# Kernel optimization log

Hardware: AMD Instinct MI355X
Metric: run time of the kernel (lower is better)

## Reference

```python
import jax, jax.numpy as jnp
import numpy as np

T_STEPS, N, STATE, HID, ACT, C = 32, 64, 64, 128, 32, 96


def setup_inputs() -> dict:
    key = jax.random.key(0)
    ks = jax.random.split(key, 16)
    s = 0.05
    inp = {
        'x': jax.random.normal(ks[0], (T_STEPS, N, STATE), jnp.float32),
        'a': jax.random.normal(ks[1], (T_STEPS, N, ACT), jnp.float32),
        # GRU layer 0 (input state_dim) and layer 1 (input hidden_dim)
        'wih0': jax.random.normal(ks[2], (3 * HID, STATE), jnp.float32) * s,
        'whh0': jax.random.normal(ks[3], (3 * HID, HID), jnp.float32) * s,
        'bih0': jax.random.normal(ks[4], (3 * HID,), jnp.float32) * s,
        'bhh0': jax.random.normal(ks[5], (3 * HID,), jnp.float32) * s,
        'wih1': jax.random.normal(ks[6], (3 * HID, HID), jnp.float32) * s,
        'whh1': jax.random.normal(ks[7], (3 * HID, HID), jnp.float32) * s,
        'bih1': jax.random.normal(ks[8], (3 * HID,), jnp.float32) * s,
        'bhh1': jax.random.normal(ks[9], (3 * HID,), jnp.float32) * s,
        'w1': jax.random.normal(ks[10], (HID, HID + ACT), jnp.float32) * s,
        'b1': jax.random.normal(ks[11], (HID,), jnp.float32) * s,
        'w2': jax.random.normal(ks[12], (1, 2 * HID), jnp.float32) * s,
        'b2': jax.random.normal(ks[13], (1,), jnp.float32) * s,
        'Tm': jax.random.normal(ks[14], (HID, HID, C), jnp.float32),  # init.normal(T,0,1)
    }
    return inp


def _gru_cell(x_t, h, wih, whh, bih, bhh):
    gi = x_t @ wih.T + bih            # (N, 3H)
    gh = h @ whh.T + bhh
    i_r, i_z, i_n = jnp.split(gi, 3, axis=-1)
    h_r, h_z, h_n = jnp.split(gh, 3, axis=-1)
    r = jax.nn.sigmoid(i_r + h_r)
    z = jax.nn.sigmoid(i_z + h_z)
    n = jnp.tanh(i_n + r * h_n)
    return (1.0 - z) * n + z * h


def reference(x, a, wih0, whh0, bih0, bhh0, wih1, whh1, bih1, bhh1, w1, b1, w2, b2, Tm):
    def step(h, x_t):
        h0 = _gru_cell(x_t, h[0], wih0, whh0, bih0, bhh0)
        h1 = _gru_cell(h0, h[1], wih1, whh1, bih1, bhh1)
        return jnp.stack([h0, h1]), h1

    h_init = jnp.zeros((2, N, HID), x.dtype)
    _, p = jax.lax.scan(step, h_init, x)              # (T, N, H)

    fc1 = jax.nn.relu(jnp.concatenate([p, a], -1) @ w1.T + b1)  # (T, N, H)

    Tflat = Tm.reshape(HID, HID * C)

    def batch_discrim(xt):  # xt: (N, H)
        M = (xt @ Tflat).reshape(N, HID, C)           # (N, B, C)
        # pairwise L1 over C: (N, N, B)
        norm = jnp.abs(M[:, None] - M[None, :]).sum(-1)
        o_b = (jnp.exp(-norm).sum(0) - 1.0) / (N - 1)  # (N, B)
        return jnp.concatenate([xt, o_b], 1)          # (N, 2H)

    fc2 = jax.lax.map(batch_discrim, fc1)             # (T, N, 2H)
    prob = jax.nn.sigmoid(fc2 @ w2.T + b2)            # (T, N, 1)
    return prob
```

## Files before the change

### kernel.cpp

```cpp
#include <hip/hip_runtime.h>
#include <hip/hip_fp16.h>
#include <cstdint>

#define T_STEPS 32
#define NB 64
#define STATE 64
#define HID 128
#define ACT 32
#define CDIM 96
#define G3 (3*HID)

typedef __attribute__((ext_vector_type(8))) short short8;
typedef __attribute__((ext_vector_type(4))) float f32x4;
typedef _Float16 h2v __attribute__((ext_vector_type(2)));

__device__ __forceinline__ unsigned short f2bf(float f){
  unsigned int u = __builtin_bit_cast(unsigned int, f);
  u = u + 0x7FFFu + ((u >> 16) & 1u);
  return (unsigned short)(u >> 16);
}
__device__ __forceinline__ float bf2f(unsigned short u){
  unsigned int v = ((unsigned int)u) << 16; return __builtin_bit_cast(float, v);
}
__device__ __forceinline__ unsigned int packh2(float f0, float f1){
  return (unsigned int)__half_as_ushort(__float2half_rn(f0)) |
         ((unsigned int)__half_as_ushort(__float2half_rn(f1)) << 16);
}
__device__ __forceinline__ float sigmoidf_(float x){ return 1.0f/(1.0f + __expf(-x)); }
__device__ __forceinline__ float tanhf_(float x){ float e = __expf(2.0f*x); return (e-1.0f)/(e+1.0f); }

__device__ __forceinline__ float dot2f(float acc, unsigned int a, unsigned int b){
  h2v av = __builtin_bit_cast(h2v, a);
  h2v bv = __builtin_bit_cast(h2v, b);
  return __builtin_amdgcn_fdot2(av, bv, acc, false);
}
__device__ __forceinline__ float l1d(float acc, unsigned int ua, unsigned int ub){
  __half2 a = __builtin_bit_cast(__half2, ua);
  __half2 b = __builtin_bit_cast(__half2, ub);
  __half2 d = __habs2(__hsub2(a, b));
  h2v dv = __builtin_bit_cast(h2v, d);
  h2v ones; ones[0] = (_Float16)1.0f; ones[1] = (_Float16)1.0f;
  return __builtin_amdgcn_fdot2(dv, ones, acc, false);
}
__device__ __forceinline__ float l1d4(float acc, uint4 a, uint4 b){
  acc = l1d(acc, a.x, b.x); acc = l1d(acc, a.y, b.y);
  acc = l1d(acc, a.z, b.z); acc = l1d(acc, a.w, b.w);
  return acc;
}

__global__ void k_prep(const float* __restrict__ Tm, unsigned short* __restrict__ tmh,
                       const float* __restrict__ whh0, const float* __restrict__ whh1,
                       const float* __restrict__ w1, const float* __restrict__ wih0,
                       const float* __restrict__ wih1, const float* __restrict__ x,
                       const float* __restrict__ a,
                       unsigned int* __restrict__ whh0p, unsigned int* __restrict__ whh1p,
                       unsigned short* __restrict__ w1f, unsigned short* __restrict__ wi0f,
                       unsigned short* __restrict__ wi1f, unsigned short* __restrict__ xaf,
                       unsigned short* __restrict__ h1af){
  int tid = threadIdx.x;
  int bx = blockIdx.x;
  if (bx < 128){
    int b = bx;
    for (int e = tid; e < HID*CDIM; e += 256){
      int chunk = e / 768;
      int r1 = e - chunk*768;
      int c = r1 >> 3, h = r1 & 7;
      int k = chunk*8 + h;
      tmh[b*(HID*CDIM) + e] = f2bf(Tm[k*(HID*CDIM) + b*CDIM + c]);
    }
  } else if (bx < 132){
    for (int e = (bx-128)*256 + tid; e < 24576; e += 1024){
      int k2 = e / 384, r = e - k2*384;
      whh0p[e] = packh2(whh0[r*128 + 2*k2], whh0[r*128 + 2*k2 + 1]);
      whh1p[e] = packh2(whh1[r*128 + 2*k2], whh1[r*128 + 2*k2 + 1]);
    }
  } else if (bx < 136){
    for (int e = (bx-132)*256 + tid; e < 20480; e += 1024){
      int kc = e >> 10, rem = e & 1023;
      int col = rem >> 3, j = rem & 7;
      w1f[e] = f2bf(w1[col*160 + kc*8 + j]);
    }
  } else if (bx < 140){
    for (int e = (bx-136)*256 + tid; e < 24576; e += 1024){
      int kc = e / 3072, rem = e - kc*3072;
      int col = rem >> 3, kl = rem & 7;
      wi0f[e] = f2bf(wih0[col*64 + kc*8 + kl]);
    }
  } else if (bx < 144){
    for (int e = (bx-140)*256 + tid; e < 49152; e += 1024){
      int kc = e / 3072, rem = e - kc*3072;
      int col = rem >> 3, kl = rem & 7;
      wi1f[e] = f2bf(wih1[col*128 + kc*8 + kl]);
    }
  } else if (bx < 156){
    for (int e = (bx-144)*256 + tid; e < 131072; e += 3072){
      int t = e >> 12, rem = e & 4095;
      int ntile = rem >> 10, rem2 = rem & 1023;
      int kc = rem2 >> 7, nl = (rem2 >> 3) & 15, kl = rem2 & 7;
      int n = ntile*16 + nl, k = kc*8 + kl;
      xaf[e] = f2bf(x[t*4096 + n*64 + k]);
    }
  } else {
    for (int e = (bx-156)*256 + tid; e < 65536; e += 3072){
      int t = e >> 11, rem = e & 2047;
      int n = rem >> 5, c = rem & 31;
      int pos = t*10240 + (n>>4)*2560 + (16 + (c>>3))*128 + (n&15)*8 + (c&7);
      h1af[pos] = f2bf(a[t*(NB*ACT) + n*ACT + c]);
    }
  }
}

template<int KK, int TSU>
__global__ __launch_bounds__(256) void k_gi(const unsigned short* __restrict__ af,
                                            const unsigned short* __restrict__ wf,
                                            const float* __restrict__ bias,
                                            float* __restrict__ gig){
  int t = blockIdx.x, by = blockIdx.y, tid = threadIdx.x;
  int wave = tid >> 6, lane = tid & 63, m = lane & 15, quad = lane >> 4;
  const uint4* A4 = (const uint4*)af;
  const uint4* B4 = (const uint4*)wf;
  uint4 av[KK];
  #pragma unroll
  for (int kk = 0; kk < KK; kk++) av[kk] = A4[t*TSU + wave*(TSU/4) + (kk*4+quad)*16 + m];
  f32x4 acc[6];
  #pragma unroll
  for (int i = 0; i < 6; i++) acc[i] = (f32x4)(0.0f);
  #pragma unroll
  for (int kk = 0; kk < KK; kk++){
    short8 a = __builtin_bit_cast(short8, av[kk]);
    #pragma unroll
    for (int ntl = 0; ntl < 6; ntl++){
      int nt = by*6 + ntl;
      uint4 bv = B4[(kk*4+quad)*384 + nt*16 + m];
      acc[ntl] = __builtin_amdgcn_mfma_f32_16x16x32_bf16(a, __builtin_bit_cast(short8, bv), acc[ntl], 0, 0, 0);
    }
  }
  #pragma unroll
  for (int ntl = 0; ntl < 6; ntl++){
    int col = (by*6+ntl)*16 + m;
    float bv = bias[col];
    #pragma unroll
    for (int rr = 0; rr < 4; rr++){
      int n = wave*16 + quad*4 + rr;
      gig[(t*NB + n)*G3 + col] = acc[ntl][rr] + bv;
    }
  }
}

template<int TS, int NS>
__global__ __launch_bounds__(768, 3) void k_rec(const unsigned int* __restrict__ whhp,
                                                const float* __restrict__ bhh,
                                                const float* __restrict__ gig,
                                                unsigned short* __restrict__ haf){
  __shared__ __align__(16) unsigned int hl[64];
  __shared__ float A0[G3];
  int n = blockIdx.x, tid = threadIdx.x;
  int r = tid >> 1, kh = tid & 1;
  unsigned int wh[32];
  #pragma unroll
  for (int i = 0; i < 32; i++) wh[i] = whhp[(kh*32 + i)*384 + r];
  float bh = (kh == 0) ? bhh[r] : 0.0f;
  if (tid < 64) hl[tid] = 0u;
  float g_r = 0.0f, g_z = 0.0f, g_n = 0.0f, hprev = 0.0f;
  if (tid < HID){
    const float* gp = gig + n*G3 + tid;
    g_r = gp[0]; g_z = gp[HID]; g_n = gp[2*HID];
  }
  __syncthreads();
  const uint4* h4 = (const uint4*)hl;
  for (int t = 0; t < T_STEPS; t++){
    float gh = bh;
    #pragma unroll
    for (int g = 0; g < 2; g++){
      uint4 hv[4];
      #pragma unroll
      for (int j = 0; j < 4; j++) hv[j] = h4[kh*8 + g*4 + j];
      #pragma unroll
      for (int j = 0; j < 4; j++){
        gh = dot2f(gh, wh[g*16 + j*4 + 0], hv[j].x);
        gh = dot2f(gh, wh[g*16 + j*4 + 1], hv[j].y);
        gh = dot2f(gh, wh[g*16 + j*4 + 2], hv[j].z);
        gh = dot2f(gh, wh[g*16 + j*4 + 3], hv[j].w);
      }
    }
    gh += __shfl_xor(gh, 1);
    if (kh == 0) A0[r] = gh;
    __syncthreads();
    if (tid < HID){
      float cr = g_r, cz = g_z, cn = g_n;
      int tn2 = (t+1 < T_STEPS) ? t+1 : t;
      const float* gp = gig + (tn2*NB + n)*G3 + tid;
      g_r = gp[0]; g_z = gp[HID]; g_n = gp[2*HID];
      float rg = sigmoidf_(cr + A0[tid]);
      float z  = sigmoidf_(cz + A0[tid+HID]);
      float nn = tanhf_   (cn + rg*A0[tid+2*HID]);
      float hn = (1.0f - z)*nn + z*hprev;
      hprev = hn;
      ((__half*)hl)[tid] = __float2half_rn(hn);
      haf[t*TS + (n>>4)*NS + (tid>>3)*128 + (n&15)*8 + (tid&7)] = f2bf(hn);
    }
    __syncthreads();
  }
}

__global__ __launch_bounds__(256) void k_fc1(const unsigned short* __restrict__ h1af,
                                             const unsigned short* __restrict__ w1f,
                                             const float* __restrict__ b1,
                                             unsigned short* __restrict__ fc1h){
  __shared__ float b1s[128];
  int t = blockIdx.x, tid = threadIdx.x;
  int wave = tid >> 6, lane = tid & 63, m = lane & 15, quad = lane >> 4;
  if (tid < 128) b1s[tid] = b1[tid];
  const uint4* A4 = (const uint4*)(h1af + t*10240);
  const uint4* B4 = (const uint4*)w1f;
  f32x4 acc[8];
  #pragma unroll
  for (int i = 0; i < 8; i++) acc[i] = (f32x4)(0.0f);
  #pragma unroll
  for (int ks = 0; ks < 5; ks++){
    uint4 av = A4[wave*320 + (ks*4 + quad)*16 + m];
    short8 avs = __builtin_bit_cast(short8, av);
    #pragma unroll
    for (int nt = 0; nt < 8; nt++){
      uint4 bv = B4[(ks*4 + quad)*128 + nt*16 + m];
      acc[nt] = __builtin_amdgcn_mfma_f32_16x16x32_bf16(avs, __builtin_bit_cast(short8, bv), acc[nt], 0, 0, 0);
    }
  }
  __syncthreads();
  #pragma unroll
  for (int nt = 0; nt < 8; nt++){
    float bj = b1s[nt*16 + m];
    #pragma unroll
    for (int rr = 0; rr < 4; rr++){
      float v = fmaxf(acc[nt][rr] + bj, 0.0f);
      fc1h[t*8192 + wave*2048 + (nt*2 + (m>>3))*128 + (quad*4 + rr)*8 + (m&7)] = f2bf(v);
    }
  }
}

__global__ __launch_bounds__(256) void k_disc(const unsigned short* __restrict__ fc1h,
                                              const unsigned short* __restrict__ tmh,
                                              float* __restrict__ O){
  __shared__ __align__(16) __half Mh[64*104];
  __shared__ float ps[64*18];
  int b = blockIdx.x;
  int tid = threadIdx.x;
  int wave = tid >> 6, lane = tid & 63, m = lane & 15, quad = lane >> 4;
  const uint4* Bg = (const uint4*)(tmh + b*(CDIM*HID));
  #pragma unroll 1
  for (int tt = 0; tt < 4; tt++){
    int t = blockIdx.y*4 + tt;
    const uint4* Ag = (const uint4*)(fc1h + t*8192);
    uint4 a4[4];
    #pragma unroll
    for (int kk = 0; kk < 4; kk++) a4[kk] = Ag[wave*256 + (kk*4 + quad)*16 + m];
    f32x4 acc[6];
    #pragma unroll
    for (int i = 0; i < 6; i++) acc[i] = (f32x4)(0.0f);
    #pragma unroll
    for (int kk = 0; kk < 4; kk++){
      short8 av = __builtin_bit_cast(short8, a4[kk]);
      #pragma unroll
      for (int nt = 0; nt < 6; nt++){
        uint4 b4 = Bg[(kk*4 + quad)*96 + nt*16 + m];
        acc[nt] = __builtin_amdgcn_mfma_f32_16x16x32_bf16(av, __builtin_bit_cast(short8, b4), acc[nt], 0, 0, 0);
      }
    }
    __syncthreads();
    #pragma unroll
    for (int nt = 0; nt < 6; nt++){
      #pragma unroll
      for (int rr = 0; rr < 4; rr++){
        Mh[(rr*16 + wave*4 + quad)*104 + nt*16 + m] = __float2half(acc[nt][rr]);
      }
    }
    __syncthreads();
    const uint4* M4 = (const uint4*)Mh;
    if (tid < 240){
      int chalf = tid & 1, tp = tid >> 1;
      int rnd = tp >> 3, slot = tp & 7;
      int ta, tb;
      if (slot == 0){ ta = 15; tb = rnd; }
      else {
        ta = rnd + slot;      if (ta >= 15) ta -= 15;
        tb = rnd + 15 - slot; if (tb >= 15) tb -= 15;
      }
      float facc[16];
      #pragma unroll
      for (int p = 0; p < 16; p++) facc[p] = 0.0f;
      auto doChunk = [&](int c){
        int ch = chalf*6 + c;
        uint4 av[4], bv[4];
        #pragma unroll
        for (int s = 0; s < 4; s++){
          av[s] = M4[(s*16 + ta)*13 + ch];
          bv[s] = M4[(s*16 + tb)*13 + ch];
        }
        #pragma unroll
        for (int i = 0; i < 4; i++)
          #pragma unroll
          for (int j = 0; j < 4; j++)
            facc[i*4+j] = l1d4(facc[i*4+j], av[i], bv[j]);
      };
      doChunk(0); doChunk(1);
      bool big1 = true;
      #pragma unroll
      for (int p = 0; p < 16; p++) big1 = big1 && (facc[p] > 14.0f);
      if (!big1){
        doChunk(2); doChunk(3);
        bool big2 = true;
        #pragma unroll
        for (int p = 0; p < 16; p++) big2 = big2 && (facc[p] > 14.0f);
        if (!big2){ doChunk(4); doChunk(5); }
      }
      float tot[16];
      #pragma unroll
      for (int p = 0; p < 16; p++) tot[p] = facc[p] + __shfl_xor(facc[p], 1);
      if (chalf == 0){
        #pragma unroll
        for (int i = 0; i < 4; i++){
          float s = 0.0f;
          #pragma unroll
          for (int j = 0; j < 4; j++) s += __expf(-tot[i*4+j]);
          ps[(ta*4 + i)*18 + tb] = s;
        }
      } else {
        #pragma unroll
        for (int j = 0; j < 4; j++){
          float s = 0.0f;
          #pragma unroll
          for (int i = 0; i < 4; i++) s += __expf(-tot[i*4+j]);
          ps[(tb*4 + j)*18 + ta] = s;
        }
      }
    } else {
      int ta = tid - 240;
      float f6[6];
      #pragma unroll
      for (int p = 0; p < 6; p++) f6[p] = 0.0f;
      auto doChunkS = [&](int ch){
        uint4 rv[4];
        #pragma unroll
        for (int s = 0; s < 4; s++) rv[s] = M4[(s*16 + ta)*13 + ch];
        f6[0] = l1d4(f6[0], rv[0], rv[1]);
        f6[1] = l1d4(f6[1], rv[0], rv[2]);
        f6[2] = l1d4(f6[2], rv[0], rv[3]);
        f6[3] = l1d4(f6[3], rv[1], rv[2]);
        f6[4] = l1d4(f6[4], rv[1], rv[3]);
        f6[5] = l1d4(f6[5], rv[2], rv[3]);
      };
      doChunkS(0); doChunkS(1); doChunkS(2);
      bool big1 = true;
      #pragma unroll
      for (int p = 0; p < 6; p++) big1 = big1 && (f6[p] > 14.0f);
      if (!big1){
        doChunkS(3); doChunkS(4); doChunkS(5);
        bool big2 = true;
        #pragma unroll
        for (int p = 0; p < 6; p++) big2 = big2 && (f6[p] > 14.0f);
        if (!big2){
          doChunkS(6); doChunkS(7); doChunkS(8);
          doChunkS(9); doChunkS(10); doChunkS(11);
        }
      }
      float e01 = __expf(-f6[0]), e02 = __expf(-f6[1]), e03 = __expf(-f6[2]);
      float e12 = __expf(-f6[3]), e13 = __expf(-f6[4]), e23 = __expf(-f6[5]);
      ps[(ta*4 + 0)*18 + ta] = e01 + e02 + e03;
      ps[(ta*4 + 1)*18 + ta] = e01 + e12 + e13;
      ps[(ta*4 + 2)*18 + ta] = e02 + e12 + e23;
      ps[(ta*4 + 3)*18 + ta] = e03 + e13 + e23;
    }
    __syncthreads();
    if (tid < NB){
      float s = 0.0f;
      #pragma unroll
      for (int k = 0; k < 16; k++) s += ps[tid*18 + k];
      O[(t*HID + b)*NB + tid] = s*(1.0f/63.0f);
    }
  }
}

__global__ __launch_bounds__(256) void k_final(const unsigned short* __restrict__ fc1h,
                                               const float* __restrict__ O,
                                               const float* __restrict__ w2, const float* __restrict__ b2,
                                               float* __restrict__ out){
  __shared__ float ol[NB*HID];
  __shared__ unsigned short fr[8192];
  __shared__ float wl[2*HID + 2];
  int t = blockIdx.x, tid = threadIdx.x;
  for (int i = tid; i < NB*HID; i += 256) ol[i] = O[t*NB*HID + i];
  const uint4* Fg = (const uint4*)(fc1h + t*8192);
  for (int i = tid; i < 1024; i += 256) ((uint4*)fr)[i] = Fg[i];
  if (tid < 2*HID) wl[tid] = w2[tid];
  if (tid == 0) wl[2*HID] = b2[0];
  __syncthreads();
  if (tid < NB){
    float acc = wl[2*HID];
    int base = (tid>>4)*2048 + (tid&15)*8;
    #pragma unroll 8
    for (int j = 0; j < HID; j++) acc += bf2f(fr[base + (j>>3)*128 + (j&7)])*wl[j];
    #pragma unroll 8
    for (int b = 0; b < HID; b++) acc += ol[b*NB + tid]*wl[HID + b];
    out[t*NB + tid] = sigmoidf_(acc);
  }
}

extern "C" void kernel_launch(void* const* d_in, const int* in_sizes, int n_in,
                              void* d_out, int out_size, void* d_ws, size_t ws_size,
                              hipStream_t stream){
  const float* x    = (const float*)d_in[0];
  const float* a    = (const float*)d_in[1];
  const float* wih0 = (const float*)d_in[2];
  const float* whh0 = (const float*)d_in[3];
  const float* bih0 = (const float*)d_in[4];
  const float* bhh0 = (const float*)d_in[5];
  const float* wih1 = (const float*)d_in[6];
  const float* whh1 = (const float*)d_in[7];
  const float* bih1 = (const float*)d_in[8];
  const float* bhh1 = (const float*)d_in[9];
  const float* w1   = (const float*)d_in[10];
  const float* b1   = (const float*)d_in[11];
  const float* w2   = (const float*)d_in[12];
  const float* b2   = (const float*)d_in[13];
  const float* Tm   = (const float*)d_in[14];
  float* ws = (float*)d_ws;
  float* Ows = ws;
  unsigned int* whh0p = (unsigned int*)(ws + 262144);
  unsigned int* whh1p = (unsigned int*)(ws + 286720);
  unsigned short* tmh  = (unsigned short*)(ws + 311296);
  unsigned short* fc1h = (unsigned short*)(ws + 1097728);
  unsigned short* h1af = (unsigned short*)(ws + 1228800);
  unsigned short* w1f  = (unsigned short*)(ws + 1392640);
  unsigned short* xaf  = (unsigned short*)(ws + 1402880);
  unsigned short* wi0f = (unsigned short*)(ws + 1468416);
  unsigned short* wi1f = (unsigned short*)(ws + 1480704);
  unsigned short* h0af = (unsigned short*)(ws + 1505280);
  float* gig = ws + 1636352;
  float* out = (float*)d_out;

  k_prep<<<dim3(168), dim3(256), 0, stream>>>(Tm, tmh, whh0, whh1, w1, wih0, wih1, x, a,
                                              whh0p, whh1p, w1f, wi0f, wi1f, xaf, h1af);
  k_gi<2, 512><<<dim3(T_STEPS, 4), dim3(256), 0, stream>>>(xaf, wi0f, bih0, gig);
  k_rec<8192, 2048><<<dim3(NB), dim3(768), 0, stream>>>(whh0p, bhh0, gig, h0af);
  k_gi<4, 1024><<<dim3(T_STEPS, 4), dim3(256), 0, stream>>>(h0af, wi1f, bih1, gig);
  k_rec<10240, 2560><<<dim3(NB), dim3(768), 0, stream>>>(whh1p, bhh1, gig, h1af);
  k_fc1<<<dim3(T_STEPS), dim3(256), 0, stream>>>(h1af, w1f, b1, fc1h);
  k_disc<<<dim3(HID, T_STEPS/4), dim3(256), 0, stream>>>(fc1h, tmh, Ows);
  k_final<<<dim3(T_STEPS), dim3(256), 0, stream>>>(fc1h, Ows, w2, b2, out);
}
```

Measured before the change: 210.2 us.

## Fuse GRU input projections into recurrent kernels and double-buffer discriminator stage

New measurement: 210.3 us. Within noise of the previous version (+0.0%).

```diff
diff --git a/kernel.cpp b/kernel.cpp
--- a/kernel.cpp
+++ b/kernel.cpp
@@ -51,12 +51,10 @@
 __global__ void k_prep(const float* __restrict__ Tm, unsigned short* __restrict__ tmh,
                        const float* __restrict__ whh0, const float* __restrict__ whh1,
                        const float* __restrict__ w1, const float* __restrict__ wih0,
-                       const float* __restrict__ wih1, const float* __restrict__ x,
-                       const float* __restrict__ a,
+                       const float* __restrict__ wih1, const float* __restrict__ a,
                        unsigned int* __restrict__ whh0p, unsigned int* __restrict__ whh1p,
-                       unsigned short* __restrict__ w1f, unsigned short* __restrict__ wi0f,
-                       unsigned short* __restrict__ wi1f, unsigned short* __restrict__ xaf,
-                       unsigned short* __restrict__ h1af){
+                       unsigned short* __restrict__ w1f, unsigned int* __restrict__ wih0p,
+                       unsigned int* __restrict__ wih1p, unsigned short* __restrict__ h1af){
   int tid = threadIdx.x;
   int bx = blockIdx.x;
   if (bx < 128){
@@ -80,28 +78,18 @@
       int col = rem >> 3, j = rem & 7;
       w1f[e] = f2bf(w1[col*160 + kc*8 + j]);
     }
-  } else if (bx < 140){
-    for (int e = (bx-136)*256 + tid; e < 24576; e += 1024){
-      int kc = e / 3072, rem = e - kc*3072;
-      int col = rem >> 3, kl = rem & 7;
-      wi0f[e] = f2bf(wih0[col*64 + kc*8 + kl]);
-    }
-  } else if (bx < 144){
-    for (int e = (bx-140)*256 + tid; e < 49152; e += 1024){
-      int kc = e / 3072, rem = e - kc*3072;
-      int col = rem >> 3, kl = rem & 7;
-      wi1f[e] = f2bf(wih1[col*128 + kc*8 + kl]);
-    }
-  } else if (bx < 156){
-    for (int e = (bx-144)*256 + tid; e < 131072; e += 3072){
-      int t = e >> 12, rem = e & 4095;
-      int ntile = rem >> 10, rem2 = rem & 1023;
-      int kc = rem2 >> 7, nl = (rem2 >> 3) & 15, kl = rem2 & 7;
-      int n = ntile*16 + nl, k = kc*8 + kl;
-      xaf[e] = f2bf(x[t*4096 + n*64 + k]);
+  } else if (bx < 138){
+    for (int e = (bx-136)*256 + tid; e < 12288; e += 512){
+      int k2 = e / 384, r = e - k2*384;
+      wih0p[e] = packh2(wih0[r*64 + 2*k2], wih0[r*64 + 2*k2 + 1]);
+    }
+  } else if (bx < 142){
+    for (int e = (bx-138)*256 + tid; e < 24576; e += 1024){
+      int k2 = e / 384, r = e - k2*384;
+      wih1p[e] = packh2(wih1[r*128 + 2*k2], wih1[r*128 + 2*k2 + 1]);
     }
   } else {
-    for (int e = (bx-156)*256 + tid; e < 65536; e += 3072){
+    for (int e = (bx-142)*256 + tid; e < 65536; e += 3072){
       int t = e >> 11, rem = e & 2047;
       int n = rem >> 5, c = rem & 31;
       int pos = t*10240 + (n>>4)*2560 + (16 + (c>>3))*128 + (n&15)*8 + (c&7);
@@ -110,66 +98,50 @@
   }
 }
 
-template<int KK, int TSU>
-__global__ __launch_bounds__(256) void k_gi(const unsigned short* __restrict__ af,
-                                            const unsigned short* __restrict__ wf,
-                                            const float* __restrict__ bias,
-                                            float* __restrict__ gig){
-  int t = blockIdx.x, by = blockIdx.y, tid = threadIdx.x;
-  int wave = tid >> 6, lane = tid & 63, m = lane & 15, quad = lane >> 4;
-  const uint4* A4 = (const uint4*)af;
-  const uint4* B4 = (const uint4*)wf;
-  uint4 av[KK];
-  #pragma unroll
-  for (int kk = 0; kk < KK; kk++) av[kk] = A4[t*TSU + wave*(TSU/4) + (kk*4+quad)*16 + m];
-  f32x4 acc[6];
-  #pragma unroll
-  for (int i = 0; i < 6; i++) acc[i] = (f32x4)(0.0f);
-  #pragma unroll
-  for (int kk = 0; kk < KK; kk++){
-    short8 a = __builtin_bit_cast(short8, av[kk]);
-    #pragma unroll
-    for (int ntl = 0; ntl < 6; ntl++){
-      int nt = by*6 + ntl;
-      uint4 bv = B4[(kk*4+quad)*384 + nt*16 + m];
-      acc[ntl] = __builtin_amdgcn_mfma_f32_16x16x32_bf16(a, __builtin_bit_cast(short8, bv), acc[ntl], 0, 0, 0);
-    }
-  }
-  #pragma unroll
-  for (int ntl = 0; ntl < 6; ntl++){
-    int col = (by*6+ntl)*16 + m;
-    float bv = bias[col];
-    #pragma unroll
-    for (int rr = 0; rr < 4; rr++){
-      int n = wave*16 + quad*4 + rr;
-      gig[(t*NB + n)*G3 + col] = acc[ntl][rr] + bv;
-    }
-  }
-}
-
-template<int TS, int NS>
-__global__ __launch_bounds__(768, 3) void k_rec(const unsigned int* __restrict__ whhp,
-                                                const float* __restrict__ bhh,
-                                                const float* __restrict__ gig,
-                                                unsigned short* __restrict__ haf){
+__global__ __launch_bounds__(768, 3) void k_rec0(const float* __restrict__ x,
+                                                 const unsigned int* __restrict__ wihp,
+                                                 const unsigned int* __restrict__ whhp,
+                                                 const float* __restrict__ bih, const float* __restrict__ bhh,
+                                                 unsigned short* __restrict__ h0g){
+  __shared__ __align__(16) unsigned int xall[1024];
   __shared__ __align__(16) unsigned int hl[64];
   __shared__ float A0[G3];
+  __shared__ float GI[2][G3];
   int n = blockIdx.x, tid = threadIdx.x;
   int r = tid >> 1, kh = tid & 1;
-  unsigned int wh[32];
+  unsigned int wh[32], wi[16];
   #pragma unroll
   for (int i = 0; i < 32; i++) wh[i] = whhp[(kh*32 + i)*384 + r];
+  #pragma unroll
+  for (int i = 0; i < 16; i++) wi[i] = wihp[(kh*16 + i)*384 + r];
   float bh = (kh == 0) ? bhh[r] : 0.0f;
+  float bi = (kh == 0) ? bih[r] : 0.0f;
+  for (int e = tid; e < 1024; e += 768){
+    int t_ = e >> 5, i = e & 31;
+    const float* xp = x + t_*(NB*STATE) + n*STATE + 2*i;
+    xall[e] = packh2(xp[0], xp[1]);
+  }
   if (tid < 64) hl[tid] = 0u;
-  float g_r = 0.0f, g_z = 0.0f, g_n = 0.0f, hprev = 0.0f;
-  if (tid < HID){
-    const float* gp = gig + n*G3 + tid;
-    g_r = gp[0]; g_z = gp[HID]; g_n = gp[2*HID];
-  }
-  __syncthreads();
-  const uint4* h4 = (const uint4*)hl;
+  float hprev = 0.0f;
+  __syncthreads();
+  const uint4* xl4 = (const uint4*)xall;
+  const uint4* h4  = (const uint4*)hl;
+  {
+    float gi = bi;
+    #pragma unroll
+    for (int j = 0; j < 4; j++){
+      uint4 xv = xl4[kh*4 + j];
+      gi = dot2f(gi, wi[j*4 + 0], xv.x);
+      gi = dot2f(gi, wi[j*4 + 1], xv.y);
+      gi = dot2f(gi, wi[j*4 + 2], xv.z);
+      gi = dot2f(gi, wi[j*4 + 3], xv.w);
+    }
+    gi += __shfl_xor(gi, 1);
+    if (kh == 0) GI[0][r] = gi;
+  }
+  __syncthreads();
   for (int t = 0; t < T_STEPS; t++){
-    float gh = bh;
+    float gh = bh, gin = bi;
     #pragma unroll
     for (int g = 0; g < 2; g++){
       uint4 hv[4];
@@ -183,21 +155,123 @@
         gh = dot2f(gh, wh[g*16 + j*4 + 3], hv[j].w);
       }
     }
-    gh += __shfl_xor(gh, 1);
-    if (kh == 0) A0[r] = gh;
+    if (t + 1 < T_STEPS){
+      #pragma unroll
+      for (int j = 0; j < 4; j++){
+        uint4 xv = xl4[(t+1)*8 + kh*4 + j];
+        gin = dot2f(gin, wi[j*4 + 0], xv.x);
+        gin = dot2f(gin, wi[j*4 + 1], xv.y);
+        gin = dot2f(gin, wi[j*4 + 2], xv.z);
+        gin = dot2f(gin, wi[j*4 + 3], xv.w);
+      }
+    }
+    gh  += __shfl_xor(gh, 1);
+    gin += __shfl_xor(gin, 1);
+    if (kh == 0){
+      A0[r] = gh;
+      if (t + 1 < T_STEPS) GI[(t+1)&1][r] = gin;
+    }
     __syncthreads();
     if (tid < HID){
-      float cr = g_r, cz = g_z, cn = g_n;
-      int tn2 = (t+1 < T_STEPS) ? t+1 : t;
-      const float* gp = gig + (tn2*NB + n)*G3 + tid;
-      g_r = gp[0]; g_z = gp[HID]; g_n = gp[2*HID];
-      float rg = sigmoidf_(cr + A0[tid]);
-      float z  = sigmoidf_(cz + A0[tid+HID]);
-      float nn = tanhf_   (cn + rg*A0[tid+2*HID]);
+      const float* gi = GI[t&1];
+      float rg = sigmoidf_(gi[tid]       + A0[tid]);
+      float z  = sigmoidf_(gi[tid+HID]   + A0[tid+HID]);
+      float nn = tanhf_   (gi[tid+2*HID] + rg*A0[tid+2*HID]);
       float hn = (1.0f - z)*nn + z*hprev;
       hprev = hn;
       ((__half*)hl)[tid] = __float2half_rn(hn);
-      haf[t*TS + (n>>4)*NS + (tid>>3)*128 + (n&15)*8 + (tid&7)] = f2bf(hn);
+      h0g[n*4096 + t*128 + tid] = __half_as_ushort(__float2half_rn(hn));
+    }
+    __syncthreads();
+  }
+}
+
+__global__ __launch_bounds__(768, 3) void k_rec1(const unsigned short* __restrict__ h0g,
+                                                 const unsigned int* __restrict__ wihp,
+                                                 const unsigned int* __restrict__ whhp,
+                                                 const float* __restrict__ bih, const float* __restrict__ bhh,
+                                                 unsigned short* __restrict__ h1af){
+  __shared__ __align__(16) unsigned int h0all[2048];
+  __shared__ __align__(16) unsigned int hl[64];
+  __shared__ float A0[G3];
+  __shared__ float GI[2][G3];
+  int n = blockIdx.x, tid = threadIdx.x;
+  int r = tid >> 1, kh = tid & 1;
+  unsigned int wh[32], wi[32];
+  #pragma unroll
+  for (int i = 0; i < 32; i++) wh[i] = whhp[(kh*32 + i)*384 + r];
+  #pragma unroll
+  for (int i = 0; i < 32; i++) wi[i] = wihp[(kh*32 + i)*384 + r];
+  float bh = (kh == 0) ? bhh[r] : 0.0f;
+  float bi = (kh == 0) ? bih[r] : 0.0f;
+  const unsigned int* h0u = (const unsigned int*)h0g;
+  for (int e = tid; e < 2048; e += 768) h0all[e] = h0u[n*2048 + e];
+  if (tid < 64) hl[tid] = 0u;
+  float hprev = 0.0f;
+  __syncthreads();
+  const uint4* h0l4 = (const uint4*)h0all;
+  const uint4* h4   = (const uint4*)hl;
+  {
+    float gi = bi;
+    #pragma unroll
+    for (int g = 0; g < 2; g++){
+      #pragma unroll
+      for (int j = 0; j < 4; j++){
+        uint4 hv = h0l4[kh*8 + g*4 + j];
+        gi = dot2f(gi, wi[g*16 + j*4 + 0], hv.x);
+        gi = dot2f(gi, wi[g*16 + j*4 + 1], hv.y);
+        gi = dot2f(gi, wi[g*16 + j*4 + 2], hv.z);
+        gi = dot2f(gi, wi[g*16 + j*4 + 3], hv.w);
+      }
+    }
+    gi += __shfl_xor(gi, 1);
+    if (kh == 0) GI[0][r] = gi;
+  }
+  __syncthreads();
+  for (int t = 0; t < T_STEPS; t++){
+    float gh = bh, gin = bi;
+    #pragma unroll
+    for (int g = 0; g < 2; g++){
+      uint4 hv[4];
+      #pragma unroll
+      for (int j = 0; j < 4; j++) hv[j] = h4[kh*8 + g*4 + j];
+      #pragma unroll
+      for (int j = 0; j < 4; j++){
+        gh = dot2f(gh, wh[g*16 + j*4 + 0], hv[j].x);
+        gh = dot2f(gh, wh[g*16 + j*4 + 1], hv[j].y);
+        gh = dot2f(gh, wh[g*16 + j*4 + 2], hv[j].z);
+        gh = dot2f(gh, wh[g*16 + j*4 + 3], hv[j].w);
+      }
+    }
+    if (t + 1 < T_STEPS){
+      #pragma unroll
+      for (int g = 0; g < 2; g++){
+        #pragma unroll
+        for (int j = 0; j < 4; j++){
+          uint4 hv = h0l4[(t+1)*16 + kh*8 + g*4 + j];
+          gin = dot2f(gin, wi[g*16 + j*4 + 0], hv.x);
+          gin = dot2f(gin, wi[g*16 + j*4 + 1], hv.y);
+          gin = dot2f(gin, wi[g*16 + j*4 + 2], hv.z);
+          gin = dot2f(gin, wi[g*16 + j*4 + 3], hv.w);
+        }
+      }
+    }
+    gh  += __shfl_xor(gh, 1);
+    gin += __shfl_xor(gin, 1);
+    if (kh == 0){
+      A0[r] = gh;
+      if (t + 1 < T_STEPS) GI[(t+1)&1][r] = gin;
+    }
+    __syncthreads();
+    if (tid < HID){
+      const float* gi = GI[t&1];
+      float rg = sigmoidf_(gi[tid]       + A0[tid]);
+      float z  = sigmoidf_(gi[tid+HID]   + A0[tid+HID]);
+      float nn = tanhf_   (gi[tid+2*HID] + rg*A0[tid+2*HID]);
+      float hn = (1.0f - z)*nn + z*hprev;
+      hprev = hn;
+      ((__half*)hl)[tid] = __float2half_rn(hn);
+      h1af[t*10240 + (n>>4)*2560 + (tid>>3)*128 + (n&15)*8 + (tid&7)] = f2bf(hn);
     }
     __syncthreads();
   }
@@ -241,19 +315,20 @@
 __global__ __launch_bounds__(256) void k_disc(const unsigned short* __restrict__ fc1h,
                                               const unsigned short* __restrict__ tmh,
                                               float* __restrict__ O){
-  __shared__ __align__(16) __half Mh[64*104];
-  __shared__ float ps[64*18];
+  __shared__ __align__(16) __half Mh[2][64*104];
+  __shared__ float ps[2][64*18];
   int b = blockIdx.x;
   int tid = threadIdx.x;
   int wave = tid >> 6, lane = tid & 63, m = lane & 15, quad = lane >> 4;
+  int t0 = blockIdx.y*4;
   const uint4* Bg = (const uint4*)(tmh + b*(CDIM*HID));
+  uint4 a4[4];
+  #pragma unroll
+  for (int kk = 0; kk < 4; kk++) a4[kk] = ((const uint4*)(fc1h + t0*8192))[wave*256 + (kk*4 + quad)*16 + m];
   #pragma unroll 1
   for (int tt = 0; tt < 4; tt++){
-    int t = blockIdx.y*4 + tt;
-    const uint4* Ag = (const uint4*)(fc1h + t*8192);
-    uint4 a4[4];
-    #pragma unroll
-    for (int kk = 0; kk < 4; kk++) a4[kk] = Ag[wave*256 + (kk*4 + quad)*16 + m];
+    int p = tt & 1;
+    int t = t0 + tt;
     f32x4 acc[6];
     #pragma unroll
     for (int i = 0; i < 6; i++) acc[i] = (f32x4)(0.0f);
@@ -266,16 +341,25 @@
         acc[nt] = __builtin_amdgcn_mfma_f32_16x16x32_bf16(av, __builtin_bit_cast(short8, b4), acc[nt], 0, 0, 0);
       }
     }
+    if (tt < 3){
+      #pragma unroll
+      for (int kk = 0; kk < 4; kk++) a4[kk] = ((const uint4*)(fc1h + (t+1)*8192))[wave*256 + (kk*4 + quad)*16 + m];
+    }
+    #pragma unroll
+    for (int nt = 0; nt < 6; nt++){
+      #pragma unroll
+      for (int rr = 0; rr < 4; rr++){
+        Mh[p][(rr*16 + wave*4 + quad)*104 + nt*16 + m] = __float2half(acc[nt][rr]);
+      }
+    }
     __syncthreads();
-    #pragma unroll
-    for (int nt = 0; nt < 6; nt++){
-      #pragma unroll
-      for (int rr = 0; rr < 4; rr++){
-        Mh[(rr*16 + wave*4 + quad)*104 + nt*16 + m] = __float2half(acc[nt][rr]);
-      }
-    }
-    __syncthreads();
-    const uint4* M4 = (const uint4*)Mh;
+    if (tt > 0 && tid < NB){
+      float s = 0.0f;
+      #pragma unroll
+      for (int k = 0; k < 16; k++) s += ps[1-p][tid*18 + k];
+      O[((t-1)*HID + b)*NB + tid] = s*(1.0f/63.0f);
+    }
+    const uint4* M4 = (const uint4*)Mh[p];
     if (tid < 240){
       int chalf = tid & 1, tp = tid >> 1;
       int rnd = tp >> 3, slot = tp & 7;
@@ -287,7 +371,7 @@
       }
       float facc[16];
       #pragma unroll
-      for (int p = 0; p < 16; p++) facc[p] = 0.0f;
+      for (int pp = 0; pp < 16; pp++) facc[pp] = 0.0f;
       auto doChunk = [&](int c){
         int ch = chalf*6 + c;
         uint4 av[4], bv[4];
@@ -305,24 +389,24 @@
       doChunk(0); doChunk(1);
       bool big1 = true;
       #pragma unroll
-      for (int p = 0; p < 16; p++) big1 = big1 && (facc[p] > 14.0f);
+      for (int pp = 0; pp < 16; pp++) big1 = big1 && (facc[pp] > 14.0f);
       if (!big1){
         doChunk(2); doChunk(3);
         bool big2 = true;
         #pragma unroll
-        for (int p = 0; p < 16; p++) big2 = big2 && (facc[p] > 14.0f);
+        for (int pp = 0; pp < 16; pp++) big2 = big2 && (facc[pp] > 14.0f);
         if (!big2){ doChunk(4); doChunk(5); }
       }
       float tot[16];
       #pragma unroll
-      for (int p = 0; p < 16; p++) tot[p] = facc[p] + __shfl_xor(facc[p], 1);
+      for (int pp = 0; pp < 16; pp++) tot[pp] = facc[pp] + __shfl_xor(facc[pp], 1);
       if (chalf == 0){
         #pragma unroll
         for (int i = 0; i < 4; i++){
           float s = 0.0f;
           #pragma unroll
           for (int j = 0; j < 4; j++) s += __expf(-tot[i*4+j]);
-          ps[(ta*4 + i)*18 + tb] = s;
+          ps[p][(ta*4 + i)*18 + tb] = s;
         }
       } else {
         #pragma unroll
@@ -330,14 +414,14 @@
           float s = 0.0f;
           #pragma unroll
           for (int i = 0; i < 4; i++) s += __expf(-tot[i*4+j]);
-          ps[(tb*4 + j)*18 + ta] = s;
+          ps[p][(tb*4 + j)*18 + ta] = s;
         }
       }
     } else {
       int ta = tid - 240;
       float f6[6];
       #pragma unroll
-      for (int p = 0; p < 6; p++) f6[p] = 0.0f;
+      for (int pp = 0; pp < 6; pp++) f6[pp] = 0.0f;
       auto doChunkS = [&](int ch){
         uint4 rv[4];
         #pragma unroll
@@ -352,12 +436,12 @@
       doChunkS(0); doChunkS(1); doChunkS(2);
       bool big1 = true;
       #pragma unroll
-      for (int p = 0; p < 6; p++) big1 = big1 && (f6[p] > 14.0f);
+      for (int pp = 0; pp < 6; pp++) big1 = big1 && (f6[pp] > 14.0f);
       if (!big1){
         doChunkS(3); doChunkS(4); doChunkS(5);
         bool big2 = true;
         #pragma unroll
-        for (int p = 0; p < 6; p++) big2 = big2 && (f6[p] > 14.0f);
+        for (int pp = 0; pp < 6; pp++) big2 = big2 && (f6[pp] > 14.0f);
         if (!big2){
           doChunkS(6); doChunkS(7); doChunkS(8);
           doChunkS(9); doChunkS(10); doChunkS(11);
@@ -365,18 +449,18 @@
       }
       float e01 = __expf(-f6[0]), e02 = __expf(-f6[1]), e03 = __expf(-f6[2]);
       float e12 = __expf(-f6[3]), e13 = __expf(-f6[4]), e23 = __expf(-f6[5]);
-      ps[(ta*4 + 0)*18 + ta] = e01 + e02 + e03;
-      ps[(ta*4 + 1)*18 + ta] = e01 + e12 + e13;
-      ps[(ta*4 + 2)*18 + ta] = e02 + e12 + e23;
-      ps[(ta*4 + 3)*18 + ta] = e03 + e13 + e23;
-    }
-    __syncthreads();
-    if (tid < NB){
-      float s = 0.0f;
-      #pragma unroll
-      for (int k = 0; k < 16; k++) s += ps[tid*18 + k];
-      O[(t*HID + b)*NB + tid] = s*(1.0f/63.0f);
-    }
+      ps[p][(ta*4 + 0)*18 + ta] = e01 + e02 + e03;
+      ps[p][(ta*4 + 1)*18 + ta] = e01 + e12 + e13;
+      ps[p][(ta*4 + 2)*18 + ta] = e02 + e12 + e23;
+      ps[p][(ta*4 + 3)*18 + ta] = e03 + e13 + e23;
+    }
+  }
+  __syncthreads();
+  if (tid < NB){
+    float s = 0.0f;
+    #pragma unroll
+    for (int k = 0; k < 16; k++) s += ps[1][tid*18 + k];
+    O[((t0+3)*HID + b)*NB + tid] = s*(1.0f/63.0f);
   }
 }
 
@@ -427,23 +511,19 @@
   float* Ows = ws;
   unsigned int* whh0p = (unsigned int*)(ws + 262144);
   unsigned int* whh1p = (unsigned int*)(ws + 286720);
-  unsigned short* tmh  = (unsigned short*)(ws + 311296);
-  unsigned short* fc1h = (unsigned short*)(ws + 1097728);
-  unsigned short* h1af = (unsigned short*)(ws + 1228800);
-  unsigned short* w1f  = (unsigned short*)(ws + 1392640);
-  unsigned short* xaf  = (unsigned short*)(ws + 1402880);
-  unsigned short* wi0f = (unsigned short*)(ws + 1468416);
-  unsigned short* wi1f = (unsigned short*)(ws + 1480704);
-  unsigned short* h0af = (unsigned short*)(ws + 1505280);
-  float* gig = ws + 1636352;
+  unsigned int* wih0p = (unsigned int*)(ws + 311296);
+  unsigned int* wih1p = (unsigned int*)(ws + 323584);
+  unsigned short* tmh  = (unsigned short*)(ws + 348160);
+  unsigned short* fc1h = (unsigned short*)(ws + 1134592);
+  unsigned short* h1af = (unsigned short*)(ws + 1265664);
+  unsigned short* w1f  = (unsigned short*)(ws + 1429504);
+  unsigned short* h0g  = (unsigned short*)(ws + 1439744);
   float* out = (float*)d_out;
 
-  k_prep<<<dim3(168), dim3(256), 0, stream>>>(Tm, tmh, whh0, whh1, w1, wih0, wih1, x, a,
-                                              whh0p, whh1p, w1f, wi0f, wi1f, xaf, h1af);
-  k_gi<2, 512><<<dim3(T_STEPS, 4), dim3(256), 0, stream>>>(xaf, wi0f, bih0, gig);
-  k_rec<8192, 2048><<<dim3(NB), dim3(768), 0, stream>>>(whh0p, bhh0, gig, h0af);
-  k_gi<4, 1024><<<dim3(T_STEPS, 4), dim3(256), 0, stream>>>(h0af, wi1f, bih1, gig);
-  k_rec<10240, 2560><<<dim3(NB), dim3(768), 0, stream>>>(whh1p, bhh1, gig, h1af);
+  k_prep<<<dim3(154), dim3(256), 0, stream>>>(Tm, tmh, whh0, whh1, w1, wih0, wih1, a,
+                                              whh0p, whh1p, w1f, wih0p, wih1p, h1af);
+  k_rec0<<<dim3(NB), dim3(768), 0, stream>>>(x, wih0p, whh0p, bih0, bhh0, h0g);
+  k_rec1<<<dim3(NB), dim3(768), 0, stream>>>(h0g, wih1p, whh1p, bih1, bhh1, h1af);
   k_fc1<<<dim3(T_STEPS), dim3(256), 0, stream>>>(h1af, w1f, b1, fc1h);
   k_disc<<<dim3(HID, T_STEPS/4), dim3(256), 0, stream>>>(fc1h, tmh, Ows);
   k_final<<<dim3(T_STEPS), dim3(256), 0, stream>>>(fc1h, Ows, w2, b2, out);
```
